# Kernel tuning notes

Hardware: AMD Instinct MI355X
Metric: run time of the kernel (lower is better)

## Reference

```python
import jax, jax.numpy as jnp
from jax import lax
import numpy as np

BETA = 0.9
SLOPE = 25.0  # snntorch fast_sigmoid default slope

@jax.custom_vjp
def spike_fn(mem_shift):
    # Heaviside forward, fast-sigmoid surrogate backward
    return (mem_shift > 0).astype(mem_shift.dtype)

def _spike_fwd(mem_shift):
    return spike_fn(mem_shift), mem_shift

def _spike_bwd(mem_shift, g):
    return (g / (SLOPE * jnp.abs(mem_shift) + 1.0) ** 2,)

spike_fn.defvjp(_spike_fwd, _spike_bwd)

def lif_step(inp, mem, thr):
    # snntorch Leaky, reset_mechanism='subtract': reset computed from PREVIOUS mem, detached
    reset = lax.stop_gradient((mem - thr > 0).astype(mem.dtype))
    mem_new = BETA * mem + inp - reset * thr  # thr keeps grad through reset term
    spk = spike_fn(mem_new - thr)
    return spk, mem_new

def _linear_init(key, out_f, in_f):
    k1, k2 = jax.random.split(key)
    bound = 1.0 / np.sqrt(in_f)
    W = jax.random.uniform(k1, (out_f, in_f), jnp.float32, -bound, bound)
    b = jax.random.uniform(k2, (out_f,), jnp.float32, -bound, bound)
    return W, b

def setup_inputs() -> dict:
    key = jax.random.key(0)
    ks = jax.random.split(key, 6)
    B, T = 2048, 112
    x = jax.random.normal(ks[0], (B, T, 4), jnp.float32)
    W1, b1 = _linear_init(ks[1], 1300, 4)
    W2, b2 = _linear_init(ks[2], 340, 1300)
    W3, b3 = _linear_init(ks[3], 1400, 340)
    W4, b4 = _linear_init(ks[4], 4, 1400)
    return {
        'x': x,
        'W1': W1, 'b1': b1, 'bias1': jnp.zeros((1300,), jnp.float32),
        'W2': W2, 'b2': b2, 'bias2': jnp.zeros((340,), jnp.float32),
        'W3': W3, 'b3': b3, 'bias3': jnp.zeros((1400,), jnp.float32),
        'W4': W4, 'b4': b4, 'bias4': jnp.zeros((4,), jnp.float32),
        'thr4': jnp.asarray(0.5, jnp.float32),
    }

def reference(x, W1, b1, bias1, W2, b2, bias2, W3, b3, bias3, W4, b4, bias4, thr4):
    B, T, _ = x.shape
    one = jnp.asarray(1.0, x.dtype)

    def step(carry, xt):
        m1, m2, m3, m4 = carry
        xt = xt / 50.0 + 0.001
        s1, m1 = lif_step(xt @ W1.T + b1 + bias1, m1, one)
        s2, m2 = lif_step(s1 @ W2.T + b2 + bias2, m2, one)
        s3, m3 = lif_step(s2 @ W3.T + b3 + bias3, m3, one)
        s4, m4 = lif_step(s3 @ W4.T + b4 + bias4, m4, thr4)
        return (m1, m2, m3, m4), s4

    init = tuple(jnp.zeros((B, d), x.dtype) for d in (1300, 340, 1400, 4))
    _, spk4 = lax.scan(step, init, jnp.swapaxes(x, 0, 1))  # [T,B,4]
    spk4_stack = jnp.swapaxes(spk4, 0, 1)  # [B,T,4]
    spike_counts = spk4_stack.sum(axis=1)  # [B,4]
    return spike_counts, spk4_stack
```

## Files before the change

### kernel.cpp

```cpp
#include <hip/hip_runtime.h>

#define B_ROWS  2048
#define T_STEPS 112
#define N1 1300
#define N2 340
#define N3 1400

#define R1 384
#define R2 96
#define R3 384

#define OFF_W2T 0
#define OFF_W3T 442000
#define OFF_W4T 918000
#define OFF_BS1 923600
#define OFF_BS2 924900
#define OFF_BS3 925240
#define OFF_BS4 926640
#define WS_FLOATS 926644

__global__ __launch_bounds__(256) void snn_prep(
    const float* __restrict__ W2, const float* __restrict__ W3, const float* __restrict__ W4,
    const float* __restrict__ b1, const float* __restrict__ bias1,
    const float* __restrict__ b2, const float* __restrict__ bias2,
    const float* __restrict__ b3, const float* __restrict__ bias3,
    const float* __restrict__ b4, const float* __restrict__ bias4,
    float* __restrict__ ws)
{
    for (int idx = blockIdx.x * blockDim.x + threadIdx.x; idx < WS_FLOATS;
         idx += gridDim.x * blockDim.x) {
        float v;
        if (idx < OFF_W3T) {
            int j = idx; int i = j / N2, k = j % N2;
            v = W2[k * N1 + i];
        } else if (idx < OFF_W4T) {
            int j = idx - OFF_W3T; int i = j / N3, k = j % N3;
            v = W3[k * N2 + i];
        } else if (idx < OFF_BS1) {
            int j = idx - OFF_W4T; int i = j / 4, k = j % 4;
            v = W4[k * N3 + i];
        } else if (idx < OFF_BS2) { int j = idx - OFF_BS1; v = b1[j] + bias1[j]; }
        else if (idx < OFF_BS3)   { int j = idx - OFF_BS2; v = b2[j] + bias2[j]; }
        else if (idx < OFF_BS4)   { int j = idx - OFF_BS3; v = b3[j] + bias3[j]; }
        else                      { int j = idx - OFF_BS4; v = b4[j] + bias4[j]; }
        ws[idx] = v;
    }
}

__device__ __forceinline__ float2 pk_add(float2 a, float2 b) {
    float2 d;
    asm("v_pk_add_f32 %0, %1, %2" : "=v"(d) : "v"(a), "v"(b));
    return d;
}
__device__ __forceinline__ void pk_acc4(float4& acc, const float4 r) {
    float2 lo = pk_add(make_float2(acc.x, acc.y), make_float2(r.x, r.y));
    float2 hi = pk_add(make_float2(acc.z, acc.w), make_float2(r.z, r.w));
    acc.x = lo.x; acc.y = lo.y; acc.z = hi.x; acc.w = hi.y;
}

__global__ __launch_bounds__(256, 3) void snn_main(
    const float* __restrict__ x,
    const float* __restrict__ W1,
    const float* __restrict__ ws,
    const float* __restrict__ thr4p,
    float* __restrict__ out)
{
    const int b    = blockIdx.x;
    const int tid  = threadIdx.x;
    const int wave = tid >> 6;
    const int lane = tid & 63;

    const float* __restrict__ W2T = ws + OFF_W2T;
    const float* __restrict__ W3T = ws + OFF_W3T;
    const float* __restrict__ W4T = ws + OFF_W4T;
    const float* __restrict__ bs1 = ws + OFF_BS1;
    const float* __restrict__ bs2 = ws + OFF_BS2;
    const float* __restrict__ bs3 = ws + OFF_BS3;
    const float* __restrict__ bs4 = ws + OFF_BS4;

    __shared__ __align__(16) float pw2[4][340];
    __shared__ __align__(16) float pw3[4][1400];
    __shared__ __align__(16) unsigned short lst1[4 * R1];
    __shared__ __align__(16) unsigned short lst2[4 * R2];
    __shared__ __align__(16) unsigned short lst3[4 * R3];
    __shared__ float h4part[4][4];

    const int c1b = (wave == 0) ? 0 : (wave == 1) ? 6 : (wave == 2) ? 11 : 16;
    const int n1  = (wave == 0) ? 6 : 5;

    float mem1[6] = {0.f,0.f,0.f,0.f,0.f,0.f};
    float mem2[2] = {0.f,0.f};
    float mem3[6] = {0.f,0.f,0.f,0.f,0.f,0.f};
    float mem4 = 0.f;
    float cnt  = 0.f;
    const float thr4 = thr4p[0];

    const float4* __restrict__ xv4 = (const float4*)x;
    const float4* __restrict__ W1v = (const float4*)W1;

    int  k1v[6]; bool val1[6]; float bsv1[6];
    #pragma unroll
    for (int u = 0; u < 6; ++u) {
        k1v[u] = (c1b + u) * 64 + lane;
        val1[u] = (u < n1) && (k1v[u] < N1);
        bsv1[u] = val1[u] ? bs1[k1v[u]] : 0.f;
    }
    const bool  has2  = (tid < 84);
    const float bs2v0 = bs2[tid];
    const float bs2v1 = has2 ? bs2[tid + 256] : 0.f;
    float bs3v[6];
    #pragma unroll
    for (int k = 0; k < 5; ++k) bs3v[k] = bs3[tid + 256 * k];
    bs3v[5] = (tid < 120) ? bs3[tid + 1280] : 0.f;
    const float bs4v = bs4[lane & 3];

    const int so2 = (lane < 21) ? 4 * lane : 80;
    const int so3 = (lane < 30) ? 4 * lane : 116;

    for (int t = 0; t < T_STEPS; ++t) {
        float4 xv = xv4[b * T_STEPS + t];
        const float x0 = xv.x / 50.0f + 0.001f;
        const float x1 = xv.y / 50.0f + 0.001f;
        const float x2 = xv.z / 50.0f + 0.001f;
        const float x3 = xv.w / 50.0f + 0.001f;

        unsigned cnt1w = 0;
        #pragma unroll
        for (int u = 0; u < 6; ++u) {
            if (u < n1) {
                float h = 0.f;
                if (val1[u]) {
                    float4 wv = W1v[k1v[u]];
                    h = bsv1[u] + wv.x * x0 + wv.y * x1 + wv.z * x2 + wv.w * x3;
                }
                float m = mem1[u];
                const float r = (m > 1.0f) ? 1.0f : 0.0f;
                m = 0.9f * m + h - r;
                mem1[u] = m;
                const bool sp = val1[u] && (m > 1.0f);
                const unsigned long long bal = __ballot(sp);
                if (sp) {
                    const int pos = (int)cnt1w + (int)__popcll(bal & ((1ull << lane) - 1ull));
                    lst1[wave * R1 + pos] = (unsigned short)k1v[u];
                }
                cnt1w += (unsigned)__popcll(bal);
            }
        }

        {
            float4 accA = {0.f,0.f,0.f,0.f};
            float4 accB = {0.f,0.f,0.f,0.f};
            const unsigned short* L = lst1 + wave * R1;
            const float* baseA = W2T + 4 * lane;
            const float* baseB = W2T + 256 + so2;
            const int n = (int)cnt1w;
            int j = 0;
            if (n >= 4) {
                ushort4 i0 = *(const ushort4*)(L);
                int o0 = (int)i0.x * N2, o1 = (int)i0.y * N2;
                int o2 = (int)i0.z * N2, o3 = (int)i0.w * N2;
                float4 rA0 = *(const float4*)(baseA + o0);
                float4 rA1 = *(const float4*)(baseA + o1);
                float4 rA2 = *(const float4*)(baseA + o2);
                float4 rA3 = *(const float4*)(baseA + o3);
                float4 rB0 = *(const float4*)(baseB + o0);
                float4 rB1 = *(const float4*)(baseB + o1);
                float4 rB2 = *(const float4*)(baseB + o2);
                float4 rB3 = *(const float4*)(baseB + o3);
                for (j = 4; j + 4 <= n; j += 4) {
                    ushort4 i1 = *(const ushort4*)(L + j);
                    const int p0 = (int)i1.x * N2, p1 = (int)i1.y * N2;
                    const int p2 = (int)i1.z * N2, p3 = (int)i1.w * N2;
                    float4 sA0 = *(const float4*)(baseA + p0);
                    float4 sA1 = *(const float4*)(baseA + p1);
                    float4 sA2 = *(const float4*)(baseA + p2);
                    float4 sA3 = *(const float4*)(baseA + p3);
                    float4 sB0 = *(const float4*)(baseB + p0);
                    float4 sB1 = *(const float4*)(baseB + p1);
                    float4 sB2 = *(const float4*)(baseB + p2);
                    float4 sB3 = *(const float4*)(baseB + p3);
                    pk_acc4(accA, rA0); pk_acc4(accB, rB0);
                    pk_acc4(accA, rA1); pk_acc4(accB, rB1);
                    pk_acc4(accA, rA2); pk_acc4(accB, rB2);
                    pk_acc4(accA, rA3); pk_acc4(accB, rB3);
                    rA0 = sA0; rA1 = sA1; rA2 = sA2; rA3 = sA3;
                    rB0 = sB0; rB1 = sB1; rB2 = sB2; rB3 = sB3;
                }
                pk_acc4(accA, rA0); pk_acc4(accB, rB0);
                pk_acc4(accA, rA1); pk_acc4(accB, rB1);
                pk_acc4(accA, rA2); pk_acc4(accB, rB2);
                pk_acc4(accA, rA3); pk_acc4(accB, rB3);
            }
            for (; j < n; ++j) {
                const int o = (int)L[j] * N2;
                float4 rA = *(const float4*)(baseA + o);
                float4 rB = *(const float4*)(baseB + o);
                pk_acc4(accA, rA); pk_acc4(accB, rB);
            }
            *(float4*)&pw2[wave][4 * lane] = accA;
            if (lane < 21) *(float4*)&pw2[wave][256 + 4 * lane] = accB;
        }
        __syncthreads();

        if (wave == 3 && t > 0) {
            float h4 = bs4v + h4part[0][lane & 3];
            h4 += h4part[1][lane & 3];
            h4 += h4part[2][lane & 3];
            h4 += h4part[3][lane & 3];
            float m4 = mem4;
            const float r4 = (m4 > thr4) ? thr4 : 0.f;
            m4 = 0.9f * m4 + h4 - r4;
            mem4 = m4;
            const float s4 = (m4 > thr4) ? 1.f : 0.f;
            if (lane < 4) {
                out[8192 + (b * T_STEPS + (t - 1)) * 4 + lane] = s4;
                cnt += s4;
            }
        }

        unsigned cnt2w = 0;
        {
            const float h0 = pw2[0][tid] + pw2[1][tid] + pw2[2][tid] + pw2[3][tid] + bs2v0;
            float m = mem2[0];
            const float r = (m > 1.0f) ? 1.0f : 0.0f;
            m = 0.9f * m + h0 - r;
            mem2[0] = m;
            const bool sp0 = (m > 1.0f);
            const unsigned long long bal0 = __ballot(sp0);
            if (sp0) {
                const int pos = (int)__popcll(bal0 & ((1ull << lane) - 1ull));
                lst2[wave * R2 + pos] = (unsigned short)tid;
            }
            cnt2w += (unsigned)__popcll(bal0);

            float h1 = 0.f;
            if (has2) h1 = pw2[0][tid+256] + pw2[1][tid+256] + pw2[2][tid+256] + pw2[3][tid+256] + bs2v1;
            float m1v = mem2[1];
            const float r1v = (m1v > 1.0f) ? 1.0f : 0.0f;
            m1v = 0.9f * m1v + h1 - r1v;
            mem2[1] = m1v;
            const bool sp1 = has2 && (m1v > 1.0f);
            const unsigned long long bal1 = __ballot(sp1);
            if (sp1) {
                const int pos = (int)cnt2w + (int)__popcll(bal1 & ((1ull << lane) - 1ull));
                lst2[wave * R2 + pos] = (unsigned short)(tid + 256);
            }
            cnt2w += (unsigned)__popcll(bal1);
        }

        {
            float4 acc3[6];
            #pragma unroll
            for (int c = 0; c < 6; ++c) acc3[c] = (float4){0.f,0.f,0.f,0.f};
            const unsigned short* L = lst2 + wave * R2;
            int j = 0;
            for (; j + 2 <= (int)cnt2w; j += 2) {
                ushort2 ii = *(const ushort2*)(L + j);
                const float* ra = W3T + (int)ii.x * N3;
                const float* rb = W3T + (int)ii.y * N3;
                float4 a0 = *(const float4*)(ra + 4*lane);
                float4 a1 = *(const float4*)(ra + 256 + 4*lane);
                float4 a2 = *(const float4*)(ra + 512 + 4*lane);
                float4 a3 = *(const float4*)(ra + 768 + 4*lane);
                float4 a4 = *(const float4*)(ra + 1024 + 4*lane);
                float4 a5 = *(const float4*)(ra + 1280 + so3);
                float4 b0 = *(const float4*)(rb + 4*lane);
                float4 b1_ = *(const float4*)(rb + 256 + 4*lane);
                float4 b2_ = *(const float4*)(rb + 512 + 4*lane);
                float4 b3_ = *(const float4*)(rb + 768 + 4*lane);
                float4 b4_ = *(const float4*)(rb + 1024 + 4*lane);
                float4 b5_ = *(const float4*)(rb + 1280 + so3);
                pk_acc4(acc3[0], a0); pk_acc4(acc3[1], a1); pk_acc4(acc3[2], a2);
                pk_acc4(acc3[3], a3); pk_acc4(acc3[4], a4); pk_acc4(acc3[5], a5);
                pk_acc4(acc3[0], b0); pk_acc4(acc3[1], b1_); pk_acc4(acc3[2], b2_);
                pk_acc4(acc3[3], b3_); pk_acc4(acc3[4], b4_); pk_acc4(acc3[5], b5_);
            }
            for (; j < (int)cnt2w; ++j) {
                const float* ra = W3T + (int)L[j] * N3;
                float4 a0 = *(const float4*)(ra + 4*lane);
                float4 a1 = *(const float4*)(ra + 256 + 4*lane);
                float4 a2 = *(const float4*)(ra + 512 + 4*lane);
                float4 a3 = *(const float4*)(ra + 768 + 4*lane);
                float4 a4 = *(const float4*)(ra + 1024 + 4*lane);
                float4 a5 = *(const float4*)(ra + 1280 + so3);
                pk_acc4(acc3[0], a0); pk_acc4(acc3[1], a1); pk_acc4(acc3[2], a2);
                pk_acc4(acc3[3], a3); pk_acc4(acc3[4], a4); pk_acc4(acc3[5], a5);
            }
            #pragma unroll
            for (int c = 0; c < 5; ++c)
                *(float4*)&pw3[wave][c * 256 + 4 * lane] = acc3[c];
            if (lane < 30) *(float4*)&pw3[wave][1280 + 4 * lane] = acc3[5];
        }
        __syncthreads();

        {
            unsigned cnt3w = 0;
            #pragma unroll
            for (int k = 0; k < 6; ++k) {
                const bool valid = (k < 5) || (tid < 120);
                const int n = tid + 256 * k;
                float h = 0.f;
                if (valid) h = pw3[0][n] + pw3[1][n] + pw3[2][n] + pw3[3][n] + bs3v[k];
                float m = mem3[k];
                const float r = (m > 1.0f) ? 1.0f : 0.0f;
                m = 0.9f * m + h - r;
                mem3[k] = m;
                const bool sp = valid && (m > 1.0f);
                const unsigned long long bal = __ballot(sp);
                if (sp) {
                    const int pos = (int)cnt3w + (int)__popcll(bal & ((1ull << lane) - 1ull));
                    lst3[wave * R3 + pos] = (unsigned short)n;
                }
                cnt3w += (unsigned)__popcll(bal);
            }
            float h4p = 0.f;
            const unsigned short* L = lst3 + wave * R3;
            const int o4 = lane & 3;
            int j = 0;
            for (; j + 4 <= (int)cnt3w; j += 4) {
                ushort4 ii = *(const ushort4*)(L + j);
                float t0 = W4T[4 * (int)ii.x + o4];
                float t1 = W4T[4 * (int)ii.y + o4];
                float t2 = W4T[4 * (int)ii.z + o4];
                float t3 = W4T[4 * (int)ii.w + o4];
                h4p += t0; h4p += t1; h4p += t2; h4p += t3;
            }
            for (; j < (int)cnt3w; ++j) h4p += W4T[4 * (int)L[j] + o4];
            if (lane < 4) h4part[wave][lane] = h4p;
        }
    }

    __syncthreads();
    if (wave == 3) {
        float h4 = bs4v + h4part[0][lane & 3];
        h4 += h4part[1][lane & 3];
        h4 += h4part[2][lane & 3];
        h4 += h4part[3][lane & 3];
        float m4 = mem4;
        const float r4 = (m4 > thr4) ? thr4 : 0.f;
        m4 = 0.9f * m4 + h4 - r4;
        const float s4 = (m4 > thr4) ? 1.f : 0.f;
        if (lane < 4) {
            out[8192 + (b * T_STEPS + (T_STEPS - 1)) * 4 + lane] = s4;
            cnt += s4;
            out[b * 4 + lane] = cnt;
        }
    }
}

extern "C" void kernel_launch(void* const* d_in, const int* in_sizes, int n_in,
                              void* d_out, int out_size, void* d_ws, size_t ws_size,
                              hipStream_t stream)
{
    const float* x     = (const float*)d_in[0];
    const float* W1    = (const float*)d_in[1];
    const float* b1    = (const float*)d_in[2];
    const float* bias1 = (const float*)d_in[3];
    const float* W2    = (const float*)d_in[4];
    const float* b2    = (const float*)d_in[5];
    const float* bias2 = (const float*)d_in[6];
    const float* W3    = (const float*)d_in[7];
    const float* b3    = (const float*)d_in[8];
    const float* bias3 = (const float*)d_in[9];
    const float* W4    = (const float*)d_in[10];
    const float* b4    = (const float*)d_in[11];
    const float* bias4 = (const float*)d_in[12];
    const float* thr4  = (const float*)d_in[13];
    float* out = (float*)d_out;
    float* ws  = (float*)d_ws;

    hipLaunchKernelGGL(snn_prep, dim3(1024), dim3(256), 0, stream,
                       W2, W3, W4, b1, bias1, b2, bias2, b3, bias3, b4, bias4, ws);
    hipLaunchKernelGGL(snn_main, dim3(B_ROWS), dim3(256), 0, stream,
                       x, W1, ws, thr4, out);
}
```

Measured before the change: 2.015 ms.

## Load-balance spike-list gathers across waves for layers 2 and 3

Each wave now publishes its spike count to shared memory. After a barrier, the combined spike lists are split evenly across the four waves, instead of each wave processing only the spikes it produced. This targets imbalance where one wave with many spikes stalls the block at the next barrier. In exchange it adds two extra __syncthreads per timestep, per-wave offset computation, and scalar ushort index loads in place of vectorized ushort4 loads.

```diff
diff --git a/kernel.cpp b/kernel.cpp
--- a/kernel.cpp
+++ b/kernel.cpp
@@ -58,6 +58,91 @@
     acc.x = lo.x; acc.y = lo.y; acc.z = hi.x; acc.w = hi.y;
 }
 
+__device__ __forceinline__ void run_gather_l2(
+    const unsigned short* L, int n,
+    const float* baseA, const float* baseB, float4& accA, float4& accB)
+{
+    int j = 0;
+    if (n >= 4) {
+        int o0 = (int)L[0] * N2, o1 = (int)L[1] * N2;
+        int o2 = (int)L[2] * N2, o3 = (int)L[3] * N2;
+        float4 rA0 = *(const float4*)(baseA + o0);
+        float4 rA1 = *(const float4*)(baseA + o1);
+        float4 rA2 = *(const float4*)(baseA + o2);
+        float4 rA3 = *(const float4*)(baseA + o3);
+        float4 rB0 = *(const float4*)(baseB + o0);
+        float4 rB1 = *(const float4*)(baseB + o1);
+        float4 rB2 = *(const float4*)(baseB + o2);
+        float4 rB3 = *(const float4*)(baseB + o3);
+        for (j = 4; j + 4 <= n; j += 4) {
+            const int p0 = (int)L[j] * N2,     p1 = (int)L[j + 1] * N2;
+            const int p2 = (int)L[j + 2] * N2, p3 = (int)L[j + 3] * N2;
+            float4 sA0 = *(const float4*)(baseA + p0);
+            float4 sA1 = *(const float4*)(baseA + p1);
+            float4 sA2 = *(const float4*)(baseA + p2);
+            float4 sA3 = *(const float4*)(baseA + p3);
+            float4 sB0 = *(const float4*)(baseB + p0);
+            float4 sB1 = *(const float4*)(baseB + p1);
+            float4 sB2 = *(const float4*)(baseB + p2);
+            float4 sB3 = *(const float4*)(baseB + p3);
+            pk_acc4(accA, rA0); pk_acc4(accB, rB0);
+            pk_acc4(accA, rA1); pk_acc4(accB, rB1);
+            pk_acc4(accA, rA2); pk_acc4(accB, rB2);
+            pk_acc4(accA, rA3); pk_acc4(accB, rB3);
+            rA0 = sA0; rA1 = sA1; rA2 = sA2; rA3 = sA3;
+            rB0 = sB0; rB1 = sB1; rB2 = sB2; rB3 = sB3;
+        }
+        pk_acc4(accA, rA0); pk_acc4(accB, rB0);
+        pk_acc4(accA, rA1); pk_acc4(accB, rB1);
+        pk_acc4(accA, rA2); pk_acc4(accB, rB2);
+        pk_acc4(accA, rA3); pk_acc4(accB, rB3);
+    }
+    for (; j < n; ++j) {
+        const int o = (int)L[j] * N2;
+        float4 rA = *(const float4*)(baseA + o);
+        float4 rB = *(const float4*)(baseB + o);
+        pk_acc4(accA, rA); pk_acc4(accB, rB);
+    }
+}
+
+__device__ __forceinline__ void run_gather_l3(
+    const unsigned short* L, int n,
+    const float* __restrict__ W3T, int lane4, int so3, float4* acc3)
+{
+    int j = 0;
+    for (; j + 2 <= n; j += 2) {
+        const float* ra = W3T + (int)L[j] * N3;
+        const float* rb = W3T + (int)L[j + 1] * N3;
+        float4 a0 = *(const float4*)(ra + lane4);
+        float4 a1 = *(const float4*)(ra + 256 + lane4);
+        float4 a2 = *(const float4*)(ra + 512 + lane4);
+        float4 a3 = *(const float4*)(ra + 768 + lane4);
+        float4 a4 = *(const float4*)(ra + 1024 + lane4);
+        float4 a5 = *(const float4*)(ra + 1280 + so3);
+        float4 b0 = *(const float4*)(rb + lane4);
+        float4 b1 = *(const float4*)(rb + 256 + lane4);
+        float4 b2 = *(const float4*)(rb + 512 + lane4);
+        float4 b3 = *(const float4*)(rb + 768 + lane4);
+        float4 b4 = *(const float4*)(rb + 1024 + lane4);
+        float4 b5 = *(const float4*)(rb + 1280 + so3);
+        pk_acc4(acc3[0], a0); pk_acc4(acc3[1], a1); pk_acc4(acc3[2], a2);
+        pk_acc4(acc3[3], a3); pk_acc4(acc3[4], a4); pk_acc4(acc3[5], a5);
+        pk_acc4(acc3[0], b0); pk_acc4(acc3[1], b1); pk_acc4(acc3[2], b2);
+        pk_acc4(acc3[3], b3); pk_acc4(acc3[4], b4); pk_acc4(acc3[5], b5);
+    }
+    for (; j < n; ++j) {
+        const float* ra = W3T + (int)L[j] * N3;
+        float4 a0 = *(const float4*)(ra + lane4);
+        float4 a1 = *(const float4*)(ra + 256 + lane4);
+        float4 a2 = *(const float4*)(ra + 512 + lane4);
+        float4 a3 = *(const float4*)(ra + 768 + lane4);
+        float4 a4 = *(const float4*)(ra + 1024 + lane4);
+        float4 a5 = *(const float4*)(ra + 1280 + so3);
+        pk_acc4(acc3[0], a0); pk_acc4(acc3[1], a1); pk_acc4(acc3[2], a2);
+        pk_acc4(acc3[3], a3); pk_acc4(acc3[4], a4); pk_acc4(acc3[5], a5);
+    }
+}
+
 __global__ __launch_bounds__(256, 3) void snn_main(
     const float* __restrict__ x,
     const float* __restrict__ W1,
@@ -83,6 +168,7 @@
     __shared__ __align__(16) unsigned short lst1[4 * R1];
     __shared__ __align__(16) unsigned short lst2[4 * R2];
     __shared__ __align__(16) unsigned short lst3[4 * R3];
+    __shared__ int wcnt1[4], wcnt2[4];
     __shared__ float h4part[4][4];
 
     const int c1b = (wave == 0) ? 0 : (wave == 1) ? 6 : (wave == 2) ? 11 : 16;
@@ -116,6 +202,7 @@
 
     const int so2 = (lane < 21) ? 4 * lane : 80;
     const int so3 = (lane < 30) ? 4 * lane : 116;
+    const int lane4 = 4 * lane;
 
     for (int t = 0; t < T_STEPS; ++t) {
         float4 xv = xv4[b * T_STEPS + t];
@@ -124,81 +211,30 @@
         const float x2 = xv.z / 50.0f + 0.001f;
         const float x3 = xv.w / 50.0f + 0.001f;
 
-        unsigned cnt1w = 0;
-        #pragma unroll
-        for (int u = 0; u < 6; ++u) {
-            if (u < n1) {
-                float h = 0.f;
-                if (val1[u]) {
-                    float4 wv = W1v[k1v[u]];
-                    h = bsv1[u] + wv.x * x0 + wv.y * x1 + wv.z * x2 + wv.w * x3;
+        {
+            unsigned cnt1w = 0;
+            #pragma unroll
+            for (int u = 0; u < 6; ++u) {
+                if (u < n1) {
+                    float h = 0.f;
+                    if (val1[u]) {
+                        float4 wv = W1v[k1v[u]];
+                        h = bsv1[u] + wv.x * x0 + wv.y * x1 + wv.z * x2 + wv.w * x3;
+                    }
+                    float m = mem1[u];
+                    const float r = (m > 1.0f) ? 1.0f : 0.0f;
+                    m = 0.9f * m + h - r;
+                    mem1[u] = m;
+                    const bool sp = val1[u] && (m > 1.0f);
+                    const unsigned long long bal = __ballot(sp);
+                    if (sp) {
+                        const int pos = (int)cnt1w + (int)__popcll(bal & ((1ull << lane) - 1ull));
+                        lst1[wave * R1 + pos] = (unsigned short)k1v[u];
+                    }
+                    cnt1w += (unsigned)__popcll(bal);
                 }
-                float m = mem1[u];
-                const float r = (m > 1.0f) ? 1.0f : 0.0f;
-                m = 0.9f * m + h - r;
-                mem1[u] = m;
-                const bool sp = val1[u] && (m > 1.0f);
-                const unsigned long long bal = __ballot(sp);
-                if (sp) {
-                    const int pos = (int)cnt1w + (int)__popcll(bal & ((1ull << lane) - 1ull));
-                    lst1[wave * R1 + pos] = (unsigned short)k1v[u];
-                }
-                cnt1w += (unsigned)__popcll(bal);
-            }
-        }
-
-        {
-            float4 accA = {0.f,0.f,0.f,0.f};
-            float4 accB = {0.f,0.f,0.f,0.f};
-            const unsigned short* L = lst1 + wave * R1;
-            const float* baseA = W2T + 4 * lane;
-            const float* baseB = W2T + 256 + so2;
-            const int n = (int)cnt1w;
-            int j = 0;
-            if (n >= 4) {
-                ushort4 i0 = *(const ushort4*)(L);
-                int o0 = (int)i0.x * N2, o1 = (int)i0.y * N2;
-                int o2 = (int)i0.z * N2, o3 = (int)i0.w * N2;
-                float4 rA0 = *(const float4*)(baseA + o0);
-                float4 rA1 = *(const float4*)(baseA + o1);
-                float4 rA2 = *(const float4*)(baseA + o2);
-                float4 rA3 = *(const float4*)(baseA + o3);
-                float4 rB0 = *(const float4*)(baseB + o0);
-                float4 rB1 = *(const float4*)(baseB + o1);
-                float4 rB2 = *(const float4*)(baseB + o2);
-                float4 rB3 = *(const float4*)(baseB + o3);
-                for (j = 4; j + 4 <= n; j += 4) {
-                    ushort4 i1 = *(const ushort4*)(L + j);
-                    const int p0 = (int)i1.x * N2, p1 = (int)i1.y * N2;
-                    const int p2 = (int)i1.z * N2, p3 = (int)i1.w * N2;
-                    float4 sA0 = *(const float4*)(baseA + p0);
-                    float4 sA1 = *(const float4*)(baseA + p1);
-                    float4 sA2 = *(const float4*)(baseA + p2);
-                    float4 sA3 = *(const float4*)(baseA + p3);
-                    float4 sB0 = *(const float4*)(baseB + p0);
-                    float4 sB1 = *(const float4*)(baseB + p1);
-                    float4 sB2 = *(const float4*)(baseB + p2);
-                    float4 sB3 = *(const float4*)(baseB + p3);
-                    pk_acc4(accA, rA0); pk_acc4(accB, rB0);
-                    pk_acc4(accA, rA1); pk_acc4(accB, rB1);
-                    pk_acc4(accA, rA2); pk_acc4(accB, rB2);
-                    pk_acc4(accA, rA3); pk_acc4(accB, rB3);
-                    rA0 = sA0; rA1 = sA1; rA2 = sA2; rA3 = sA3;
-                    rB0 = sB0; rB1 = sB1; rB2 = sB2; rB3 = sB3;
-                }
-                pk_acc4(accA, rA0); pk_acc4(accB, rB0);
-                pk_acc4(accA, rA1); pk_acc4(accB, rB1);
-                pk_acc4(accA, rA2); pk_acc4(accB, rB2);
-                pk_acc4(accA, rA3); pk_acc4(accB, rB3);
-            }
-            for (; j < n; ++j) {
-                const int o = (int)L[j] * N2;
-                float4 rA = *(const float4*)(baseA + o);
-                float4 rB = *(const float4*)(baseB + o);
-                pk_acc4(accA, rA); pk_acc4(accB, rB);
-            }
-            *(float4*)&pw2[wave][4 * lane] = accA;
-            if (lane < 21) *(float4*)&pw2[wave][256 + 4 * lane] = accB;
+            }
+            if (lane == 0) wcnt1[wave] = (int)cnt1w;
         }
         __syncthreads();
 
@@ -218,8 +254,35 @@
             }
         }
 
-        unsigned cnt2w = 0;
         {
+            const int cA = wcnt1[0], cB = wcnt1[1], cC = wcnt1[2], cD = wcnt1[3];
+            int offs[5];
+            offs[0] = 0; offs[1] = cA; offs[2] = cA + cB;
+            offs[3] = offs[2] + cC; offs[4] = offs[3] + cD;
+            const int tot = offs[4];
+            const int per = (tot + 3) >> 2;
+            int gs = wave * per; if (gs > tot) gs = tot;
+            int ge = gs + per;   if (ge > tot) ge = tot;
+
+            float4 accA = {0.f,0.f,0.f,0.f};
+            float4 accB = {0.f,0.f,0.f,0.f};
+            const float* baseA = W2T + lane4;
+            const float* baseB = W2T + 256 + so2;
+            #pragma unroll
+            for (int w = 0; w < 4; ++w) {
+                const int s = (gs > offs[w]) ? gs : offs[w];
+                const int e = (ge < offs[w + 1]) ? ge : offs[w + 1];
+                if (s < e)
+                    run_gather_l2(lst1 + w * R1 + (s - offs[w]), e - s,
+                                  baseA, baseB, accA, accB);
+            }
+            *(float4*)&pw2[wave][lane4] = accA;
+            if (lane < 21) *(float4*)&pw2[wave][256 + lane4] = accB;
+        }
+        __syncthreads();
+
+        {
+            unsigned cnt2w = 0;
             const float h0 = pw2[0][tid] + pw2[1][tid] + pw2[2][tid] + pw2[3][tid] + bs2v0;
             float m = mem2[0];
             const float r = (m > 1.0f) ? 1.0f : 0.0f;
@@ -246,50 +309,35 @@
                 lst2[wave * R2 + pos] = (unsigned short)(tid + 256);
             }
             cnt2w += (unsigned)__popcll(bal1);
-        }
+            if (lane == 0) wcnt2[wave] = (int)cnt2w;
+        }
+        __syncthreads();
 
         {
+            const int cA = wcnt2[0], cB = wcnt2[1], cC = wcnt2[2], cD = wcnt2[3];
+            int offs[5];
+            offs[0] = 0; offs[1] = cA; offs[2] = cA + cB;
+            offs[3] = offs[2] + cC; offs[4] = offs[3] + cD;
+            const int tot = offs[4];
+            const int per = (tot + 3) >> 2;
+            int gs = wave * per; if (gs > tot) gs = tot;
+            int ge = gs + per;   if (ge > tot) ge = tot;
+
             float4 acc3[6];
             #pragma unroll
             for (int c = 0; c < 6; ++c) acc3[c] = (float4){0.f,0.f,0.f,0.f};
-            const unsigned short* L = lst2 + wave * R2;
-            int j = 0;
-            for (; j + 2 <= (int)cnt2w; j += 2) {
-                ushort2 ii = *(const ushort2*)(L + j);
-                const float* ra = W3T + (int)ii.x * N3;
-                const float* rb = W3T + (int)ii.y * N3;
-                float4 a0 = *(const float4*)(ra + 4*lane);
-                float4 a1 = *(const float4*)(ra + 256 + 4*lane);
-                float4 a2 = *(const float4*)(ra + 512 + 4*lane);
-                float4 a3 = *(const float4*)(ra + 768 + 4*lane);
-                float4 a4 = *(const float4*)(ra + 1024 + 4*lane);
-                float4 a5 = *(const float4*)(ra + 1280 + so3);
-                float4 b0 = *(const float4*)(rb + 4*lane);
-                float4 b1_ = *(const float4*)(rb + 256 + 4*lane);
-                float4 b2_ = *(const float4*)(rb + 512 + 4*lane);
-                float4 b3_ = *(const float4*)(rb + 768 + 4*lane);
-                float4 b4_ = *(const float4*)(rb + 1024 + 4*lane);
-                float4 b5_ = *(const float4*)(rb + 1280 + so3);
-                pk_acc4(acc3[0], a0); pk_acc4(acc3[1], a1); pk_acc4(acc3[2], a2);
-                pk_acc4(acc3[3], a3); pk_acc4(acc3[4], a4); pk_acc4(acc3[5], a5);
-                pk_acc4(acc3[0], b0); pk_acc4(acc3[1], b1_); pk_acc4(acc3[2], b2_);
-                pk_acc4(acc3[3], b3_); pk_acc4(acc3[4], b4_); pk_acc4(acc3[5], b5_);
-            }
-            for (; j < (int)cnt2w; ++j) {
-                const float* ra = W3T + (int)L[j] * N3;
-                float4 a0 = *(const float4*)(ra + 4*lane);
-                float4 a1 = *(const float4*)(ra + 256 + 4*lane);
-                float4 a2 = *(const float4*)(ra + 512 + 4*lane);
-                float4 a3 = *(const float4*)(ra + 768 + 4*lane);
-                float4 a4 = *(const float4*)(ra + 1024 + 4*lane);
-                float4 a5 = *(const float4*)(ra + 1280 + so3);
-                pk_acc4(acc3[0], a0); pk_acc4(acc3[1], a1); pk_acc4(acc3[2], a2);
-                pk_acc4(acc3[3], a3); pk_acc4(acc3[4], a4); pk_acc4(acc3[5], a5);
+            #pragma unroll
+            for (int w = 0; w < 4; ++w) {
+                const int s = (gs > offs[w]) ? gs : offs[w];
+                const int e = (ge < offs[w + 1]) ? ge : offs[w + 1];
+                if (s < e)
+                    run_gather_l3(lst2 + w * R2 + (s - offs[w]), e - s,
+                                  W3T, lane4, so3, acc3);
             }
             #pragma unroll
             for (int c = 0; c < 5; ++c)
-                *(float4*)&pw3[wave][c * 256 + 4 * lane] = acc3[c];
-            if (lane < 30) *(float4*)&pw3[wave][1280 + 4 * lane] = acc3[5];
+                *(float4*)&pw3[wave][c * 256 + lane4] = acc3[c];
+            if (lane < 30) *(float4*)&pw3[wave][1280 + lane4] = acc3[5];
         }
         __syncthreads();
 
```

New measurement: 2.135 ms. 1.06x slower.

## Double block size to 8 waves per batch row, splitting neuron work finer

Applied to the files above, without the earlier changes.

Launches 512 threads per batch row instead of 256. Each wave now owns half as many layer-1 and layer-3 neurons, and each layer-2 neuron gets one thread. The per-wave partial sums in shared memory grow to 8 slices and the reductions sum 8 partials. The intent is more parallelism and latency hiding per row with fewer registers per thread. The costs are twice the shared memory for partials, an 8-way reduction, and smaller per-wave spike-list capacity, which could overflow if spikes are dense.

```diff
diff --git a/kernel.cpp b/kernel.cpp
--- a/kernel.cpp
+++ b/kernel.cpp
@@ -6,9 +6,9 @@
 #define N2 340
 #define N3 1400
 
-#define R1 384
-#define R2 96
-#define R3 384
+#define R1 192
+#define R2 64
+#define R3 192
 
 #define OFF_W2T 0
 #define OFF_W3T 442000
@@ -58,7 +58,7 @@
     acc.x = lo.x; acc.y = lo.y; acc.z = hi.x; acc.w = hi.y;
 }
 
-__global__ __launch_bounds__(256, 3) void snn_main(
+__global__ __launch_bounds__(512, 4) void snn_main(
     const float* __restrict__ x,
     const float* __restrict__ W1,
     const float* __restrict__ ws,
@@ -78,19 +78,19 @@
     const float* __restrict__ bs3 = ws + OFF_BS3;
     const float* __restrict__ bs4 = ws + OFF_BS4;
 
-    __shared__ __align__(16) float pw2[4][340];
-    __shared__ __align__(16) float pw3[4][1400];
-    __shared__ __align__(16) unsigned short lst1[4 * R1];
-    __shared__ __align__(16) unsigned short lst2[4 * R2];
-    __shared__ __align__(16) unsigned short lst3[4 * R3];
-    __shared__ float h4part[4][4];
-
-    const int c1b = (wave == 0) ? 0 : (wave == 1) ? 6 : (wave == 2) ? 11 : 16;
-    const int n1  = (wave == 0) ? 6 : 5;
-
-    float mem1[6] = {0.f,0.f,0.f,0.f,0.f,0.f};
-    float mem2[2] = {0.f,0.f};
-    float mem3[6] = {0.f,0.f,0.f,0.f,0.f,0.f};
+    __shared__ __align__(16) float pw2[8][340];
+    __shared__ __align__(16) float pw3[8][1400];
+    __shared__ __align__(16) unsigned short lst1[8 * R1];
+    __shared__ __align__(16) unsigned short lst2[8 * R2];
+    __shared__ __align__(16) unsigned short lst3[8 * R3];
+    __shared__ float h4part[8][4];
+
+    const int c1b = (wave < 5) ? 3 * wave : 15 + 2 * (wave - 5);
+    const int n1  = (wave < 5) ? 3 : 2;
+
+    float mem1[3] = {0.f,0.f,0.f};
+    float mem2 = 0.f;
+    float mem3[3] = {0.f,0.f,0.f};
     float mem4 = 0.f;
     float cnt  = 0.f;
     const float thr4 = thr4p[0];
@@ -98,20 +98,20 @@
     const float4* __restrict__ xv4 = (const float4*)x;
     const float4* __restrict__ W1v = (const float4*)W1;
 
-    int  k1v[6]; bool val1[6]; float bsv1[6];
+    int  k1v[3]; bool val1[3]; float bsv1[3];
     #pragma unroll
-    for (int u = 0; u < 6; ++u) {
+    for (int u = 0; u < 3; ++u) {
         k1v[u] = (c1b + u) * 64 + lane;
         val1[u] = (u < n1) && (k1v[u] < N1);
         bsv1[u] = val1[u] ? bs1[k1v[u]] : 0.f;
     }
-    const bool  has2  = (tid < 84);
-    const float bs2v0 = bs2[tid];
-    const float bs2v1 = has2 ? bs2[tid + 256] : 0.f;
-    float bs3v[6];
-    #pragma unroll
-    for (int k = 0; k < 5; ++k) bs3v[k] = bs3[tid + 256 * k];
-    bs3v[5] = (tid < 120) ? bs3[tid + 1280] : 0.f;
+    const bool  act2 = (tid < N2);
+    const float bs2v = act2 ? bs2[tid] : 0.f;
+    const bool  act3hi = (tid < 376);
+    float bs3v[3];
+    bs3v[0] = bs3[tid];
+    bs3v[1] = bs3[tid + 512];
+    bs3v[2] = act3hi ? bs3[tid + 1024] : 0.f;
     const float bs4v = bs4[lane & 3];
 
     const int so2 = (lane < 21) ? 4 * lane : 80;
@@ -126,7 +126,7 @@
 
         unsigned cnt1w = 0;
         #pragma unroll
-        for (int u = 0; u < 6; ++u) {
+        for (int u = 0; u < 3; ++u) {
             if (u < n1) {
                 float h = 0.f;
                 if (val1[u]) {
@@ -202,11 +202,10 @@
         }
         __syncthreads();
 
-        if (wave == 3 && t > 0) {
-            float h4 = bs4v + h4part[0][lane & 3];
-            h4 += h4part[1][lane & 3];
-            h4 += h4part[2][lane & 3];
-            h4 += h4part[3][lane & 3];
+        if (wave == 7 && t > 0) {
+            float h4 = bs4v;
+            #pragma unroll
+            for (int p = 0; p < 8; ++p) h4 += h4part[p][lane & 3];
             float m4 = mem4;
             const float r4 = (m4 > thr4) ? thr4 : 0.f;
             m4 = 0.9f * m4 + h4 - r4;
@@ -220,32 +219,22 @@
 
         unsigned cnt2w = 0;
         {
-            const float h0 = pw2[0][tid] + pw2[1][tid] + pw2[2][tid] + pw2[3][tid] + bs2v0;
-            float m = mem2[0];
+            float h0 = 0.f;
+            if (act2) {
+                h0 = pw2[0][tid] + pw2[1][tid] + pw2[2][tid] + pw2[3][tid]
+                   + pw2[4][tid] + pw2[5][tid] + pw2[6][tid] + pw2[7][tid] + bs2v;
+            }
+            float m = mem2;
             const float r = (m > 1.0f) ? 1.0f : 0.0f;
             m = 0.9f * m + h0 - r;
-            mem2[0] = m;
-            const bool sp0 = (m > 1.0f);
+            mem2 = m;
+            const bool sp0 = act2 && (m > 1.0f);
             const unsigned long long bal0 = __ballot(sp0);
             if (sp0) {
                 const int pos = (int)__popcll(bal0 & ((1ull << lane) - 1ull));
                 lst2[wave * R2 + pos] = (unsigned short)tid;
             }
-            cnt2w += (unsigned)__popcll(bal0);
-
-            float h1 = 0.f;
-            if (has2) h1 = pw2[0][tid+256] + pw2[1][tid+256] + pw2[2][tid+256] + pw2[3][tid+256] + bs2v1;
-            float m1v = mem2[1];
-            const float r1v = (m1v > 1.0f) ? 1.0f : 0.0f;
-            m1v = 0.9f * m1v + h1 - r1v;
-            mem2[1] = m1v;
-            const bool sp1 = has2 && (m1v > 1.0f);
-            const unsigned long long bal1 = __ballot(sp1);
-            if (sp1) {
-                const int pos = (int)cnt2w + (int)__popcll(bal1 & ((1ull << lane) - 1ull));
-                lst2[wave * R2 + pos] = (unsigned short)(tid + 256);
-            }
-            cnt2w += (unsigned)__popcll(bal1);
+            cnt2w = (unsigned)__popcll(bal0);
         }
 
         {
@@ -296,11 +285,14 @@
         {
             unsigned cnt3w = 0;
             #pragma unroll
-            for (int k = 0; k < 6; ++k) {
-                const bool valid = (k < 5) || (tid < 120);
-                const int n = tid + 256 * k;
+            for (int k = 0; k < 3; ++k) {
+                const bool valid = (k < 2) || act3hi;
+                const int n = tid + 512 * k;
                 float h = 0.f;
-                if (valid) h = pw3[0][n] + pw3[1][n] + pw3[2][n] + pw3[3][n] + bs3v[k];
+                if (valid) {
+                    h = pw3[0][n] + pw3[1][n] + pw3[2][n] + pw3[3][n]
+                      + pw3[4][n] + pw3[5][n] + pw3[6][n] + pw3[7][n] + bs3v[k];
+                }
                 float m = mem3[k];
                 const float r = (m > 1.0f) ? 1.0f : 0.0f;
                 m = 0.9f * m + h - r;
@@ -331,11 +323,10 @@
     }
 
     __syncthreads();
-    if (wave == 3) {
-        float h4 = bs4v + h4part[0][lane & 3];
-        h4 += h4part[1][lane & 3];
-        h4 += h4part[2][lane & 3];
-        h4 += h4part[3][lane & 3];
+    if (wave == 7) {
+        float h4 = bs4v;
+        #pragma unroll
+        for (int p = 0; p < 8; ++p) h4 += h4part[p][lane & 3];
         float m4 = mem4;
         const float r4 = (m4 > thr4) ? thr4 : 0.f;
         m4 = 0.9f * m4 + h4 - r4;
@@ -371,6 +362,6 @@
 
     hipLaunchKernelGGL(snn_prep, dim3(1024), dim3(256), 0, stream,
                        W2, W3, W4, b1, bias1, b2, bias2, b3, bias3, b4, bias4, ws);
-    hipLaunchKernelGGL(snn_main, dim3(B_ROWS), dim3(256), 0, stream,
+    hipLaunchKernelGGL(snn_main, dim3(B_ROWS), dim3(512), 0, stream,
                        x, W1, ws, thr4, out);
 }
```

After: 2.350 ms. 1.17x slower.
